# Optimization experiments

Hardware: AMD Instinct MI355X
Metric: run time of the kernel (lower is better)

Reference implementation:

```python
import jax, jax.numpy as jnp
import numpy as np

N, E, B, D, L = 100000, 600000, 128, 128, 3
BOT = 64
EPS = 1e-5


def _forward(query_x, corpus_x, gin_eps, mlp_W1, mlp_b1, mlp_W2, mlp_b2, bn_gamma, bn_beta,
             pool_G1, pool_g1b, pool_G2, pool_g2b, pool_Wm,
             int_G1, int_g1b, int_G2, int_g2b, int_F1, int_f1b, int_F2, int_f2b,
             sc_G1, sc_g1b, sc_G2, sc_g2b, sc_F1, sc_f1b, sc_F2, sc_f2b,
             query_edge_index, query_graph_idx, corpus_edge_index, corpus_graph_idx, num_graphs):
    def gin(x, ei, l):
        # GINConv: sum of source-node features into targets, plus (1+eps)*self
        agg = jax.ops.segment_sum(x[ei[0]], ei[1], num_segments=x.shape[0])
        h = (1.0 + gin_eps[l]) * x + agg
        h = jax.nn.relu(h @ mlp_W1[l] + mlp_b1[l]) @ mlp_W2[l] + mlp_b2[l]
        mu = h.mean(axis=0)
        var = ((h - mu) ** 2).mean(axis=0)  # biased var (BatchNorm training mode)
        h = (h - mu) * jax.lax.rsqrt(var + EPS) * bn_gamma[l] + bn_beta[l]
        return jax.nn.relu(h)  # dropout p=0.0

    def pool(x, gidx, l):
        coef = jnp.tanh(jax.nn.relu(x @ pool_G1[l] + pool_g1b[l]) @ pool_G2[l] + pool_g2b[l])
        s = (coef + 1.0) * x
        sums = jax.ops.segment_sum(s, gidx, num_segments=num_graphs)
        cnt = jax.ops.segment_sum(jnp.ones((x.shape[0],), x.dtype), gidx, num_segments=num_graphs)
        mean = sums / cnt[:, None]
        gc = jnp.tanh(mean @ pool_Wm[l])  # [B, D]
        node_coef = jax.nn.sigmoid(jnp.sum(s * gc[gidx], axis=1))  # [N]
        return jax.ops.segment_sum(node_coef[:, None] * s, gidx, num_segments=num_graphs)

    def interact(q, c, l):
        comb = jnp.concatenate([q, c], axis=1)  # [B, 2D]
        coef = jax.nn.sigmoid(jax.nn.relu(comb @ int_G1[l] + int_g1b[l]) @ int_G2[l] + int_g2b[l])
        sc = (coef + 1.0) * comb
        return jax.nn.relu(jax.nn.relu(sc @ int_F1[l] + int_f1b[l]) @ int_F2[l] + int_f2b[l])

    qx, cx = query_x, corpus_x
    feats = []
    for l in range(gin_eps.shape[0]):
        qx = gin(qx, query_edge_index, l)
        cx = gin(cx, corpus_edge_index, l)
        feats.append(interact(pool(qx, query_graph_idx, l), pool(cx, corpus_graph_idx, l), l))
    f = jnp.concatenate(feats, axis=1)  # [B, sum(filters)//2]
    coef = jax.nn.sigmoid(jax.nn.relu(f @ sc_G1 + sc_g1b) @ sc_G2 + sc_g2b)
    sf = (coef + 1.0) * f
    return (jax.nn.relu(sf @ sc_F1 + sc_f1b) @ sc_F2 + sc_f2b).squeeze(-1)  # [B]


def setup_inputs() -> dict:
    key = jax.random.key(0)
    kit = iter(jax.random.split(key, 64))
    def nrm(shape, s=0.05):
        return jax.random.normal(next(kit), shape, jnp.float32) * s
    C, R, OUT, AGG, RG = 2 * D, (2 * D) // 4, D // 2, (3 * D) // 2, ((3 * D) // 2) // 4
    inp = {
        "query_x": nrm((N, D), 1.0),
        "query_edge_index": jax.random.randint(next(kit), (2, E), 0, N),
        "query_graph_idx": jnp.sort(jax.random.randint(next(kit), (N,), 0, B)),
        "corpus_x": nrm((N, D), 1.0),
        "corpus_edge_index": jax.random.randint(next(kit), (2, E), 0, N),
        "corpus_graph_idx": jnp.sort(jax.random.randint(next(kit), (N,), 0, B)),
        "num_graphs": B,
        "gin_eps": jnp.zeros((L,), jnp.float32),
        "mlp_W1": nrm((L, D, D)), "mlp_b1": jnp.zeros((L, D)),
        "mlp_W2": nrm((L, D, D)), "mlp_b2": jnp.zeros((L, D)),
        "bn_gamma": jnp.ones((L, D)), "bn_beta": jnp.zeros((L, D)),
        "pool_G1": nrm((L, D, D // 4)), "pool_g1b": jnp.zeros((L, D // 4)),
        "pool_G2": nrm((L, D // 4, D)), "pool_g2b": jnp.zeros((L, D)),
        "pool_Wm": nrm((L, D, D)),
        "int_G1": nrm((L, C, R)), "int_g1b": jnp.zeros((L, R)),
        "int_G2": nrm((L, R, C)), "int_g2b": jnp.zeros((L, C)),
        "int_F1": nrm((L, C, C)), "int_f1b": jnp.zeros((L, C)),
        "int_F2": nrm((L, C, OUT)), "int_f2b": jnp.zeros((L, OUT)),
        "sc_G1": nrm((AGG, RG)), "sc_g1b": jnp.zeros((RG,)),
        "sc_G2": nrm((RG, AGG)), "sc_g2b": jnp.zeros((AGG,)),
        "sc_F1": nrm((AGG, BOT)), "sc_f1b": jnp.zeros((BOT,)),
        "sc_F2": nrm((BOT, 1)), "sc_f2b": jnp.zeros((1,)),
    }
    return inp


def reference(query_x, query_edge_index, query_graph_idx, corpus_x, corpus_edge_index, corpus_graph_idx,
              num_graphs, gin_eps, mlp_W1, mlp_b1, mlp_W2, mlp_b2, bn_gamma, bn_beta,
              pool_G1, pool_g1b, pool_G2, pool_g2b, pool_Wm,
              int_G1, int_g1b, int_G2, int_g2b, int_F1, int_f1b, int_F2, int_f2b,
              sc_G1, sc_g1b, sc_G2, sc_g2b, sc_F1, sc_f1b, sc_F2, sc_f2b):
    return _forward(query_x, corpus_x, gin_eps, mlp_W1, mlp_b1, mlp_W2, mlp_b2, bn_gamma, bn_beta,
                    pool_G1, pool_g1b, pool_G2, pool_g2b, pool_Wm,
                    int_G1, int_g1b, int_G2, int_g2b, int_F1, int_f1b, int_F2, int_f2b,
                    sc_G1, sc_g1b, sc_G2, sc_g2b, sc_F1, sc_f1b, sc_F2, sc_f2b,
                    query_edge_index, query_graph_idx, corpus_edge_index, corpus_graph_idx, num_graphs)
```

## Files before the change

kernel.cpp:

```cpp
#include <hip/hip_runtime.h>
#include <hip/hip_bf16.h>

constexpr int NN  = 100000;
constexpr int NN2 = 200000;
constexpr int NE  = 600000;
constexpr int NB  = 128;
constexpr int D   = 128;
constexpr int NL  = 3;
constexpr int CAP = 48;
constexpr int MT_TOT = NN2 / 16;
constexpr int MT_Q   = NN / 16;

constexpr int PREP_CSR   = (2 * NE + 255) / 256;
constexpr int PREP_WPREP = 1956;
constexpr int PREP_CNT   = 64;
constexpr int PREP_TOT   = PREP_CSR + PREP_WPREP + PREP_CNT;

constexpr int NCSEG_BLK = 1024;

typedef __bf16 bf16x8 __attribute__((ext_vector_type(8)));
typedef float f32x4 __attribute__((ext_vector_type(4)));
typedef unsigned short us8 __attribute__((ext_vector_type(8)));

__device__ __forceinline__ float sigmoidf_(float x) { return 1.0f / (1.0f + __expf(-x)); }
__device__ __forceinline__ unsigned short f2b(float f) {
    __hip_bfloat16 h = __float2bfloat16(f);
    return __builtin_bit_cast(unsigned short, h);
}
__device__ __forceinline__ float b2f(unsigned short u) {
    __hip_bfloat16 h = __builtin_bit_cast(__hip_bfloat16, u);
    return __bfloat162float(h);
}
__device__ __forceinline__ bf16x8 ldfrag(const unsigned short* p) {
    return __builtin_bit_cast(bf16x8, *(const us8*)p);
}

__device__ __forceinline__ void ncseg_body(int vbid, int nstream_blocks,
                                           const unsigned short* __restrict__ S,
                                           const int* __restrict__ gq, const int* __restrict__ gc,
                                           const float* __restrict__ gcb,
                                           float* __restrict__ dq, float* __restrict__ dc) {
    int stream = vbid * 4 + (threadIdx.x >> 6);
    int lane = threadIdx.x & 63;
    int nstream = nstream_blocks * 4;
    int per = (NN2 + nstream - 1) / nstream;
    int r0 = stream * per;
    int r1 = min(r0 + per, NN2);
    if (r0 >= r1) return;
    float a0 = 0.f, a1 = 0.f;
    int cur = (r0 < NN) ? gq[r0] : 128 + gc[r0 - NN];
    for (int r = r0; r < r1; ++r) {
        int g = (r < NN) ? gq[r] : 128 + gc[r - NN];
        if (g != cur) {
            float* base = (cur < 128) ? (dq + cur * D) : (dc + (cur - 128) * D);
            atomicAdd(&base[lane * 2], a0);
            atomicAdd(&base[lane * 2 + 1], a1);
            a0 = 0.f; a1 = 0.f; cur = g;
        }
        ushort2 sv = *(const ushort2*)&S[(size_t)r * D + lane * 2];
        float2 gv = *(const float2*)&gcb[(size_t)g * D + lane * 2];
        float v0 = b2f(sv.x), v1 = b2f(sv.y);
        float p = v0 * gv.x + v1 * gv.y;
#pragma unroll
        for (int off = 1; off < 64; off <<= 1) p += __shfl_xor(p, off, 64);
        float nc = sigmoidf_(p);
        a0 += nc * v0; a1 += nc * v1;
    }
    float* base = (cur < 128) ? (dq + cur * D) : (dc + (cur - 128) * D);
    atomicAdd(&base[lane * 2], a0);
    atomicAdd(&base[lane * 2 + 1], a1);
}

__device__ __forceinline__ void gather_bf16_body(int vbid,
                                                 const unsigned short* __restrict__ xb,
                                                 unsigned short* __restrict__ z,
                                                 const int* __restrict__ deg, const int* __restrict__ bucket,
                                                 float e) {
    int r = vbid * 16 + (threadIdx.x >> 4);
    int c8 = threadIdx.x & 15;
    float a[8];
    us8 v = *(const us8*)(xb + (size_t)r * D + c8 * 8);
#pragma unroll
    for (int j = 0; j < 8; ++j) a[j] = e * b2f(v[j]);
    int d = deg[r]; d = (d < CAP) ? d : CAP;
    const int* bk = bucket + (size_t)r * CAP;
    int i = 0;
    for (; i + 4 <= d; i += 4) {
        int s0 = bk[i], s1 = bk[i + 1], s2 = bk[i + 2], s3 = bk[i + 3];
        us8 u0 = *(const us8*)(xb + (size_t)s0 * D + c8 * 8);
        us8 u1 = *(const us8*)(xb + (size_t)s1 * D + c8 * 8);
        us8 u2 = *(const us8*)(xb + (size_t)s2 * D + c8 * 8);
        us8 u3 = *(const us8*)(xb + (size_t)s3 * D + c8 * 8);
#pragma unroll
        for (int j = 0; j < 8; ++j)
            a[j] += b2f(u0[j]) + b2f(u1[j]) + b2f(u2[j]) + b2f(u3[j]);
    }
    for (; i < d; ++i) {
        int s0 = bk[i];
        us8 u0 = *(const us8*)(xb + (size_t)s0 * D + c8 * 8);
#pragma unroll
        for (int j = 0; j < 8; ++j) a[j] += b2f(u0[j]);
    }
    us8 o;
#pragma unroll
    for (int j = 0; j < 8; ++j) o[j] = f2b(a[j]);
    *(us8*)(z + (size_t)r * D + c8 * 8) = o;
}

__global__ __launch_bounds__(256) void k_prep(
    const int* __restrict__ qei, const int* __restrict__ cei,
    int* __restrict__ deg, int* __restrict__ bucket,
    const float* mW1, const float* mW2, const float* pG1, const float* pG2,
    const float* iG1, const float* iG2, const float* iF1, const float* iF2,
    const float* sG1, const float* sG2, const float* sF1,
    unsigned short* W1t, unsigned short* W2t, unsigned short* G1t, unsigned short* G2t,
    unsigned short* iG1t, unsigned short* iG2t, unsigned short* iF1t, unsigned short* iF2t,
    unsigned short* sG1t, unsigned short* sG2t, unsigned short* sF1t,
    const int* __restrict__ gq, const int* __restrict__ gc, float* __restrict__ cnt) {
    if (blockIdx.x < PREP_CSR) {
        int e = blockIdx.x * 256 + threadIdx.x;
        int src, dst;
        if (e < NE) {
            src = qei[e]; dst = qei[NE + e];
        } else if (e < 2 * NE) {
            src = cei[e - NE] + NN; dst = cei[NE + (e - NE)] + NN;
        } else return;
        int pos = atomicAdd(&deg[dst], 1);
        if (pos < CAP) bucket[(size_t)dst * CAP + pos] = src;
        return;
    }
    if (blockIdx.x < PREP_CSR + PREP_WPREP) {
        int i = (blockIdx.x - PREP_CSR) * 256 + threadIdx.x;
#define SEG(CNT, KK, NN_, SRC, DST)                                              \
        if (i < (CNT)) {                                                         \
            int l = i / ((KK) * (NN_)), r = i % ((KK) * (NN_));                  \
            int n = r / (KK), k = r % (KK);                                      \
            DST[i] = f2b(SRC[(size_t)l * (KK) * (NN_) + (size_t)k * (NN_) + n]); \
            return;                                                              \
        }                                                                        \
        i -= (CNT);
        SEG(49152, 128, 128, mW1, W1t)
        SEG(49152, 128, 128, mW2, W2t)
        SEG(12288, 128, 32, pG1, G1t)
        SEG(12288, 32, 128, pG2, G2t)
        SEG(49152, 256, 64, iG1, iG1t)
        SEG(49152, 64, 256, iG2, iG2t)
        SEG(196608, 256, 256, iF1, iF1t)
        SEG(49152, 256, 64, iF2, iF2t)
        SEG(9216, 192, 48, sG1, sG1t)
        if (i < 12288) {
            int n = i / 64, k = i % 64;
            sG2t[i] = (k < 48) ? f2b(sG2[(size_t)k * 192 + n]) : (unsigned short)0;
            return;
        }
        i -= 12288;
        SEG(12288, 192, 64, sF1, sF1t)
#undef SEG
        return;
    }
    {
        __shared__ float h[256];
        int vb = blockIdx.x - (PREP_CSR + PREP_WPREP);
        for (int i = threadIdx.x; i < 256; i += 256) h[i] = 0.f;
        __syncthreads();
        int total = PREP_CNT * 256;
        int tid = vb * 256 + threadIdx.x;
        int per = (NN2 + total - 1) / total;
        int r0 = tid * per, r1 = min(r0 + per, NN2);
        if (r0 < r1) {
            int cur = (r0 < NN) ? gq[r0] : 128 + gc[r0 - NN];
            float c = 0.f;
            for (int r = r0; r < r1; ++r) {
                int g = (r < NN) ? gq[r] : 128 + gc[r - NN];
                if (g != cur) { atomicAdd(&h[cur], c); c = 0.f; cur = g; }
                c += 1.f;
            }
            atomicAdd(&h[cur], c);
        }
        __syncthreads();
        for (int i = threadIdx.x; i < 256; i += 256)
            if (h[i] != 0.f) atomicAdd(&cnt[i], h[i]);
    }
}

__global__ __launch_bounds__(256) void k_gather0(const float* __restrict__ qx, const float* __restrict__ cx,
                                                 unsigned short* __restrict__ z,
                                                 const int* __restrict__ deg, const int* __restrict__ bucket,
                                                 const float* __restrict__ eps_p) {
    int r = blockIdx.x * 16 + (threadIdx.x >> 4);
    int c8 = threadIdx.x & 15;
    float e = 1.0f + eps_p[0];
    float a[8];
    const float* base = (r < NN) ? qx : cx;
    int off = (r < NN) ? 0 : NN;
    float4 v0 = *(const float4*)(base + (size_t)(r - off) * D + c8 * 8);
    float4 v1 = *(const float4*)(base + (size_t)(r - off) * D + c8 * 8 + 4);
    a[0] = e * v0.x; a[1] = e * v0.y; a[2] = e * v0.z; a[3] = e * v0.w;
    a[4] = e * v1.x; a[5] = e * v1.y; a[6] = e * v1.z; a[7] = e * v1.w;
    int d = deg[r]; d = (d < CAP) ? d : CAP;
    const int* bk = bucket + (size_t)r * CAP;
    int i = 0;
    for (; i + 4 <= d; i += 4) {
        int s0 = bk[i], s1 = bk[i + 1], s2 = bk[i + 2], s3 = bk[i + 3];
        const float* p0 = base + (size_t)(s0 - off) * D + c8 * 8;
        const float* p1 = base + (size_t)(s1 - off) * D + c8 * 8;
        const float* p2 = base + (size_t)(s2 - off) * D + c8 * 8;
        const float* p3 = base + (size_t)(s3 - off) * D + c8 * 8;
        float4 w0 = *(const float4*)p0, w0b = *(const float4*)(p0 + 4);
        float4 w1 = *(const float4*)p1, w1b = *(const float4*)(p1 + 4);
        float4 w2 = *(const float4*)p2, w2b = *(const float4*)(p2 + 4);
        float4 w3 = *(const float4*)p3, w3b = *(const float4*)(p3 + 4);
        a[0] += w0.x + w1.x + w2.x + w3.x; a[1] += w0.y + w1.y + w2.y + w3.y;
        a[2] += w0.z + w1.z + w2.z + w3.z; a[3] += w0.w + w1.w + w2.w + w3.w;
        a[4] += w0b.x + w1b.x + w2b.x + w3b.x; a[5] += w0b.y + w1b.y + w2b.y + w3b.y;
        a[6] += w0b.z + w1b.z + w2b.z + w3b.z; a[7] += w0b.w + w1b.w + w2b.w + w3b.w;
    }
    for (; i < d; ++i) {
        int s0 = bk[i];
        const float* p0 = base + (size_t)(s0 - off) * D + c8 * 8;
        float4 w0 = *(const float4*)p0, w0b = *(const float4*)(p0 + 4);
        a[0] += w0.x; a[1] += w0.y; a[2] += w0.z; a[3] += w0.w;
        a[4] += w0b.x; a[5] += w0b.y; a[6] += w0b.z; a[7] += w0b.w;
    }
    us8 o;
#pragma unroll
    for (int j = 0; j < 8; ++j) o[j] = f2b(a[j]);
    *(us8*)(z + (size_t)r * D + c8 * 8) = o;
}

__global__ __launch_bounds__(256) void k_gncseg(const unsigned short* __restrict__ xb,
                                                unsigned short* __restrict__ z,
                                                const int* __restrict__ deg, const int* __restrict__ bucket,
                                                const float* __restrict__ eps_p, int l,
                                                const unsigned short* __restrict__ S,
                                                const int* __restrict__ gq, const int* __restrict__ gcix,
                                                const float* __restrict__ gcb,
                                                float* __restrict__ dq, float* __restrict__ dc) {
    if (blockIdx.x < NCSEG_BLK) {
        ncseg_body(blockIdx.x, NCSEG_BLK, S, gq, gcix, gcb, dq, dc);
    } else {
        float e = 1.0f + eps_p[l];
        gather_bf16_body(blockIdx.x - NCSEG_BLK, xb, z, deg, bucket, e);
    }
}

__global__ __launch_bounds__(256) void k_ncseg(const unsigned short* __restrict__ S,
                                               const int* __restrict__ gq, const int* __restrict__ gc,
                                               const float* __restrict__ gcb,
                                               float* __restrict__ dq, float* __restrict__ dc) {
    ncseg_body(blockIdx.x, NCSEG_BLK, S, gq, gc, gcb, dq, dc);
}

constexpr int HSTR = 136;
__global__ __launch_bounds__(256, 2) void k_mlp(unsigned short* zh,
                                                const unsigned short* __restrict__ W1t,
                                                const unsigned short* __restrict__ W2t,
                                                const float* __restrict__ b1,
                                                const float* __restrict__ b2,
                                                float* __restrict__ stat) {
    __shared__ unsigned short hb[2][2][16 * HSTR];
    __shared__ float red[512];
    int wave = threadIdx.x >> 6, lane = threadIdx.x & 63;
    int col16 = lane & 15, quad = lane >> 4;
    int g = wave >> 1, half = wave & 1;
    bf16x8 bf1[4][4], bf2[4][4];
    float bb1[4], bb2[4];
#pragma unroll
    for (int t = 0; t < 4; ++t) {
        int c = half * 64 + t * 16 + col16;
        bb1[t] = b1[c]; bb2[t] = b2[c];
#pragma unroll
        for (int kc = 0; kc < 4; ++kc) {
            bf1[t][kc] = ldfrag(W1t + (size_t)c * D + kc * 32 + quad * 8);
            bf2[t][kc] = ldfrag(W2t + (size_t)c * D + kc * 32 + quad * 8);
        }
    }
    float cs[2][4] = {{0.f,0.f,0.f,0.f},{0.f,0.f,0.f,0.f}};
    float cq[2][4] = {{0.f,0.f,0.f,0.f},{0.f,0.f,0.f,0.f}};
    int groups = gridDim.x * 2;
    int iters = (MT_TOT + groups - 1) / groups;
    bf16x8 zf[4];
    {
        int mt = blockIdx.x * 2 + g;
        const unsigned short* Ap = zh + ((size_t)((mt < MT_TOT) ? mt : 0) * 16 + col16) * D + quad * 8;
#pragma unroll
        for (int kc = 0; kc < 4; ++kc) zf[kc] = ldfrag(Ap + kc * 32);
    }
    for (int n = 0; n < iters; ++n) {
        int mt = blockIdx.x * 2 + g + n * groups;
        bool act = (mt < MT_TOT);
        int pp = n & 1;
        unsigned short* hbuf = hb[pp][g];
        bf16x8 zn[4];
        {
            int mtn = blockIdx.x * 2 + g + (n + 1) * groups;
            const unsigned short* Apn = zh + ((size_t)((mtn < MT_TOT) ? mtn : 0) * 16 + col16) * D + quad * 8;
#pragma unroll
            for (int kc = 0; kc < 4; ++kc) zn[kc] = ldfrag(Apn + kc * 32);
        }
        {
            f32x4 acc[4];
#pragma unroll
            for (int t = 0; t < 4; ++t) acc[t] = (f32x4){0.f, 0.f, 0.f, 0.f};
#pragma unroll
            for (int kc = 0; kc < 4; ++kc) {
#pragma unroll
                for (int t = 0; t < 4; ++t)
                    acc[t] = __builtin_amdgcn_mfma_f32_16x16x32_bf16(zf[kc], bf1[t][kc], acc[t], 0, 0, 0);
            }
#pragma unroll
            for (int t = 0; t < 4; ++t) {
                int c = half * 64 + t * 16 + col16;
#pragma unroll
                for (int r = 0; r < 4; ++r)
                    hbuf[(quad * 4 + r) * HSTR + c] = f2b(fmaxf(acc[t][r] + bb1[t], 0.f));
            }
        }
        __syncthreads();
        {
            f32x4 acc[4];
#pragma unroll
            for (int t = 0; t < 4; ++t) acc[t] = (f32x4){0.f, 0.f, 0.f, 0.f};
#pragma unroll
            for (int kc = 0; kc < 4; ++kc) {
                bf16x8 af = ldfrag(&hbuf[col16 * HSTR + kc * 32 + quad * 8]);
#pragma unroll
                for (int t = 0; t < 4; ++t)
                    acc[t] = __builtin_amdgcn_mfma_f32_16x16x32_bf16(af, bf2[t][kc], acc[t], 0, 0, 0);
            }
            if (act) {
                int side = (mt < MT_Q) ? 0 : 1;
#pragma unroll
                for (int t = 0; t < 4; ++t) {
                    int c = half * 64 + t * 16 + col16;
#pragma unroll
                    for (int r = 0; r < 4; ++r) {
                        int m = mt * 16 + quad * 4 + r;
                        float v = acc[t][r] + bb2[t];
                        zh[(size_t)m * D + c] = f2b(v);
                        cs[side][t] += v; cq[side][t] += v * v;
                    }
                }
            }
        }
#pragma unroll
        for (int kc = 0; kc < 4; ++kc) zf[kc] = zn[kc];
    }
    for (int i = threadIdx.x; i < 512; i += 256) red[i] = 0.f;
    __syncthreads();
#pragma unroll
    for (int t = 0; t < 4; ++t) {
        int c = half * 64 + t * 16 + col16;
#pragma unroll
        for (int side = 0; side < 2; ++side) {
            atomicAdd(&red[side * 256 + c], cs[side][t]);
            atomicAdd(&red[side * 256 + 128 + c], cq[side][t]);
        }
    }
    __syncthreads();
    for (int i = threadIdx.x; i < 512; i += 256) atomicAdd(&stat[i], red[i]);
}

__global__ __launch_bounds__(256, 3) void k_pool(const unsigned short* __restrict__ H,
                                                 const unsigned short* __restrict__ G1t,
                                                 const unsigned short* __restrict__ G2t,
                                                 const float* __restrict__ b1,
                                                 const float* __restrict__ b2,
                                                 const float* __restrict__ stat,
                                                 const float* __restrict__ gamma,
                                                 const float* __restrict__ beta,
                                                 const int* __restrict__ gq, const int* __restrict__ gcix,
                                                 unsigned short* __restrict__ Xo,
                                                 unsigned short* __restrict__ S,
                                                 float* __restrict__ seg_sum) {
    __shared__ float sc_s[256], sh_s[256];
    __shared__ unsigned short xt[4][16 * HSTR];
    __shared__ unsigned short t2t[4][16 * 40];
    {
        int t = threadIdx.x, side = t >> 7, c = t & 127;
        const float invN = 1.0f / (float)NN;
        float mu = stat[side * 256 + c] * invN;
        float var = fmaxf(stat[side * 256 + 128 + c] * invN - mu * mu, 0.f);
        float inv = rsqrtf(var + 1e-5f);
        float s = gamma[c] * inv;
        sc_s[t] = s;
        sh_s[t] = beta[c] - mu * s;
    }
    __syncthreads();
    int wave = threadIdx.x >> 6, lane = threadIdx.x & 63;
    int col16 = lane & 15, quad = lane >> 4;
    unsigned short* xtile = xt[wave];
    unsigned short* t2tile = t2t[wave];
    int nwaves = gridDim.x * 4;
    int per = (MT_TOT + nwaves - 1) / nwaves;
    int wid = blockIdx.x * 4 + wave;
    int mt0 = wid * per, mt1 = min(mt0 + per, MT_TOT);
    if (mt0 >= mt1) return;

    float bb1[2], bb2[8];
#pragma unroll
    for (int t = 0; t < 2; ++t) bb1[t] = b1[t * 16 + col16];
#pragma unroll
    for (int t = 0; t < 8; ++t) bb2[t] = b2[t * 16 + col16];
    float sacc[8] = {0.f, 0.f, 0.f, 0.f, 0.f, 0.f, 0.f, 0.f};
    int curg = -1;
    for (int mt = mt0; mt < mt1; ++mt) {
        int side = (mt < MT_Q) ? 0 : 1;
        const float* scp = sc_s + side * 128;
        const float* shp = sh_s + side * 128;
        const unsigned short* Hp = H + ((size_t)mt * 16 + col16) * D + quad * 8;
        unsigned short* Xp = Xo + ((size_t)mt * 16 + col16) * D + quad * 8;
        f32x4 acc1[2];
#pragma unroll
        for (int t = 0; t < 2; ++t) acc1[t] = (f32x4){0.f, 0.f, 0.f, 0.f};
#pragma unroll
        for (int kc = 0; kc < 4; ++kc) {
            us8 hv = *(const us8*)(Hp + kc * 32);
            int k0 = kc * 32 + quad * 8;
            float4 s0 = *(const float4*)&scp[k0], s1 = *(const float4*)&scp[k0 + 4];
            float4 h0 = *(const float4*)&shp[k0], h1 = *(const float4*)&shp[k0 + 4];
            us8 xv;
            xv[0] = f2b(fmaxf(b2f(hv[0]) * s0.x + h0.x, 0.f));
            xv[1] = f2b(fmaxf(b2f(hv[1]) * s0.y + h0.y, 0.f));
            xv[2] = f2b(fmaxf(b2f(hv[2]) * s0.z + h0.z, 0.f));
            xv[3] = f2b(fmaxf(b2f(hv[3]) * s0.w + h0.w, 0.f));
            xv[4] = f2b(fmaxf(b2f(hv[4]) * s1.x + h1.x, 0.f));
            xv[5] = f2b(fmaxf(b2f(hv[5]) * s1.y + h1.y, 0.f));
            xv[6] = f2b(fmaxf(b2f(hv[6]) * s1.z + h1.z, 0.f));
            xv[7] = f2b(fmaxf(b2f(hv[7]) * s1.w + h1.w, 0.f));
            *(us8*)(Xp + kc * 32) = xv;
            *(us8*)(xtile + col16 * HSTR + k0) = xv;
            bf16x8 af = __builtin_bit_cast(bf16x8, xv);
#pragma unroll
            for (int t = 0; t < 2; ++t) {
                bf16x8 wf = ldfrag(G1t + (size_t)(t * 16 + col16) * D + kc * 32 + quad * 8);
                acc1[t] = __builtin_amdgcn_mfma_f32_16x16x32_bf16(af, wf, acc1[t], 0, 0, 0);
            }
        }
#pragma unroll
        for (int t = 0; t < 2; ++t) {
            int c = t * 16 + col16;
#pragma unroll
            for (int r = 0; r < 4; ++r)
                t2tile[(quad * 4 + r) * 40 + c] = f2b(fmaxf(acc1[t][r] + bb1[t], 0.f));
        }
        bf16x8 af2 = ldfrag(t2tile + col16 * 40 + quad * 8);
        f32x4 acc2[8];
#pragma unroll
        for (int t = 0; t < 8; ++t) {
            bf16x8 wf = ldfrag(G2t + (size_t)(t * 16 + col16) * 32 + quad * 8);
            acc2[t] = (f32x4){0.f, 0.f, 0.f, 0.f};
            acc2[t] = __builtin_amdgcn_mfma_f32_16x16x32_bf16(af2, wf, acc2[t], 0, 0, 0);
        }
#pragma unroll
        for (int r = 0; r < 4; ++r) {
            int m = mt * 16 + quad * 4 + r;
            int g = (m < NN) ? gq[m] : 128 + gcix[m - NN];
            if (g != curg) {
                if (curg >= 0) {
#pragma unroll
                    for (int t = 0; t < 8; ++t) {
                        atomicAdd(&seg_sum[(size_t)curg * D + t * 16 + col16], sacc[t]);
                        sacc[t] = 0.f;
                    }
                }
                curg = g;
            }
#pragma unroll
            for (int t = 0; t < 8; ++t) {
                int c = t * 16 + col16;
                float v = (tanhf(acc2[t][r] + bb2[t]) + 1.f) * b2f(xtile[(quad * 4 + r) * HSTR + c]);
                S[(size_t)m * D + c] = f2b(v);
                sacc[t] += v;
            }
        }
    }
    if (curg >= 0) {
#pragma unroll
        for (int t = 0; t < 8; ++t)
            atomicAdd(&seg_sum[(size_t)curg * D + t * 16 + col16], sacc[t]);
    }
}

__global__ void k_gc(float* __restrict__ sums, const float* __restrict__ cnt,
                     const float* __restrict__ Wm, float* __restrict__ gc) {
    __shared__ float m[D];
    int b = blockIdx.x, j = threadIdx.x;
    m[j] = sums[b * D + j] / cnt[b];
    sums[b * D + j] = 0.f;
    __syncthreads();
    float a = 0.f;
#pragma unroll 8
    for (int i = 0; i < D; ++i) a += m[i] * Wm[i * D + j];
    gc[b * D + j] = tanhf(a);
}

constexpr int LSTR = 264;
__global__ __launch_bounds__(256) void k_interact(const float* __restrict__ pooled,
                                                  const unsigned short* __restrict__ iG1t, const float* __restrict__ ig1b,
                                                  const unsigned short* __restrict__ iG2t, const float* __restrict__ ig2b,
                                                  const unsigned short* __restrict__ iF1t, const float* __restrict__ if1b,
                                                  const unsigned short* __restrict__ iF2t, const float* __restrict__ if2b,
                                                  unsigned short* __restrict__ featsb) {
    __shared__ unsigned short bufC[16 * LSTR];
    __shared__ unsigned short bufA[16 * LSTR];
    __shared__ unsigned short bufB[16 * LSTR];
    int t = threadIdx.x, wave = t >> 6, lane = t & 63;
    int col16 = lane & 15, quad = lane >> 4;
    int pg = blockIdx.x & 7, l = blockIdx.x >> 3;
    int p0 = pg * 16;
    {
        int r = t >> 4, c0 = (t & 15) * 16;
        const float* src = (c0 < 128)
            ? (pooled + (size_t)l * NB * D + (size_t)(p0 + r) * D + c0)
            : (pooled + (size_t)(NL + l) * NB * D + (size_t)(p0 + r) * D + (c0 - 128));
#pragma unroll
        for (int j = 0; j < 16; ++j) bufC[r * LSTR + c0 + j] = f2b(src[j]);
    }
    __syncthreads();
    {
        f32x4 acc = (f32x4){0.f, 0.f, 0.f, 0.f};
        int n = wave * 16 + col16;
#pragma unroll
        for (int kc = 0; kc < 8; ++kc) {
            bf16x8 af = ldfrag(&bufC[col16 * LSTR + kc * 32 + quad * 8]);
            bf16x8 bfr = ldfrag(iG1t + ((size_t)l * 64 + n) * 256 + kc * 32 + quad * 8);
            acc = __builtin_amdgcn_mfma_f32_16x16x32_bf16(af, bfr, acc, 0, 0, 0);
        }
        float bb = ig1b[(size_t)l * 64 + n];
#pragma unroll
        for (int r = 0; r < 4; ++r)
            bufA[(quad * 4 + r) * LSTR + n] = f2b(fmaxf(acc[r] + bb, 0.f));
    }
    __syncthreads();
    {
        f32x4 acc[4];
#pragma unroll
        for (int tt = 0; tt < 4; ++tt) acc[tt] = (f32x4){0.f, 0.f, 0.f, 0.f};
#pragma unroll
        for (int kc = 0; kc < 2; ++kc) {
            bf16x8 af = ldfrag(&bufA[col16 * LSTR + kc * 32 + quad * 8]);
#pragma unroll
            for (int tt = 0; tt < 4; ++tt) {
                int n = wave * 64 + tt * 16 + col16;
                bf16x8 bfr = ldfrag(iG2t + ((size_t)l * 256 + n) * 64 + kc * 32 + quad * 8);
                acc[tt] = __builtin_amdgcn_mfma_f32_16x16x32_bf16(af, bfr, acc[tt], 0, 0, 0);
            }
        }
#pragma unroll
        for (int tt = 0; tt < 4; ++tt) {
            int n = wave * 64 + tt * 16 + col16;
            float bb = ig2b[(size_t)l * 256 + n];
#pragma unroll
            for (int r = 0; r < 4; ++r) {
                int row = quad * 4 + r;
                float s = (sigmoidf_(acc[tt][r] + bb) + 1.f) * b2f(bufC[row * LSTR + n]);
                bufB[row * LSTR + n] = f2b(s);
            }
        }
    }
    __syncthreads();
    {
        f32x4 acc[4];
#pragma unroll
        for (int tt = 0; tt < 4; ++tt) acc[tt] = (f32x4){0.f, 0.f, 0.f, 0.f};
#pragma unroll
        for (int kc = 0; kc < 8; ++kc) {
            bf16x8 af = ldfrag(&bufB[col16 * LSTR + kc * 32 + quad * 8]);
#pragma unroll
            for (int tt = 0; tt < 4; ++tt) {
                int n = wave * 64 + tt * 16 + col16;
                bf16x8 bfr = ldfrag(iF1t + (size_t)l * 256 * 256 + (size_t)n * 256 + kc * 32 + quad * 8);
                acc[tt] = __builtin_amdgcn_mfma_f32_16x16x32_bf16(af, bfr, acc[tt], 0, 0, 0);
            }
        }
#pragma unroll
        for (int tt = 0; tt < 4; ++tt) {
            int n = wave * 64 + tt * 16 + col16;
            float bb = if1b[(size_t)l * 256 + n];
#pragma unroll
            for (int r = 0; r < 4; ++r)
                bufA[(quad * 4 + r) * LSTR + n] = f2b(fmaxf(acc[tt][r] + bb, 0.f));
        }
    }
    __syncthreads();
    {
        f32x4 acc = (f32x4){0.f, 0.f, 0.f, 0.f};
        int n = wave * 16 + col16;
#pragma unroll
        for (int kc = 0; kc < 8; ++kc) {
            bf16x8 af = ldfrag(&bufA[col16 * LSTR + kc * 32 + quad * 8]);
            bf16x8 bfr = ldfrag(iF2t + ((size_t)l * 64 + n) * 256 + kc * 32 + quad * 8);
            acc = __builtin_amdgcn_mfma_f32_16x16x32_bf16(af, bfr, acc, 0, 0, 0);
        }
        float bb = if2b[(size_t)l * 64 + n];
#pragma unroll
        for (int r = 0; r < 4; ++r)
            featsb[(size_t)(p0 + quad * 4 + r) * 192 + l * 64 + n] = f2b(fmaxf(acc[r] + bb, 0.f));
    }
}

__global__ __launch_bounds__(256) void k_score(const unsigned short* __restrict__ featsb,
                                               const unsigned short* __restrict__ sG1t, const float* __restrict__ sg1b,
                                               const unsigned short* __restrict__ sG2t, const float* __restrict__ sg2b,
                                               const unsigned short* __restrict__ sF1t, const float* __restrict__ sf1b,
                                               const float* __restrict__ sF2, const float* __restrict__ sf2b,
                                               float* __restrict__ out) {
    __shared__ unsigned short bufF[16 * 200];
    __shared__ unsigned short bufA[16 * LSTR];
    __shared__ unsigned short bufB[16 * LSTR];
    __shared__ float redf[16 * 65];
    int t = threadIdx.x, wave = t >> 6, lane = t & 63;
    int col16 = lane & 15, quad = lane >> 4;
    int p0 = blockIdx.x * 16;
    {
        int r = t >> 4, c0 = (t & 15) * 12;
#pragma unroll
        for (int j = 0; j < 12; ++j)
            bufF[r * 200 + c0 + j] = featsb[(size_t)(p0 + r) * 192 + c0 + j];
    }
    __syncthreads();
    if (wave < 3) {
        f32x4 acc = (f32x4){0.f, 0.f, 0.f, 0.f};
        int n = wave * 16 + col16;
#pragma unroll
        for (int kc = 0; kc < 6; ++kc) {
            bf16x8 af = ldfrag(&bufF[col16 * 200 + kc * 32 + quad * 8]);
            bf16x8 bfr = ldfrag(sG1t + (size_t)n * 192 + kc * 32 + quad * 8);
            acc = __builtin_amdgcn_mfma_f32_16x16x32_bf16(af, bfr, acc, 0, 0, 0);
        }
        float bb = sg1b[n];
#pragma unroll
        for (int r = 0; r < 4; ++r)
            bufA[(quad * 4 + r) * LSTR + n] = f2b(fmaxf(acc[r] + bb, 0.f));
    } else {
        int row = lane >> 2, c = 48 + (lane & 3) * 4;
#pragma unroll
        for (int j = 0; j < 4; ++j) bufA[row * LSTR + c + j] = 0;
    }
    __syncthreads();
    {
        f32x4 acc[3];
#pragma unroll
        for (int tt = 0; tt < 3; ++tt) acc[tt] = (f32x4){0.f, 0.f, 0.f, 0.f};
#pragma unroll
        for (int kc = 0; kc < 2; ++kc) {
            bf16x8 af = ldfrag(&bufA[col16 * LSTR + kc * 32 + quad * 8]);
#pragma unroll
            for (int tt = 0; tt < 3; ++tt) {
                int n = wave * 48 + tt * 16 + col16;
                bf16x8 bfr = ldfrag(sG2t + (size_t)n * 64 + kc * 32 + quad * 8);
                acc[tt] = __builtin_amdgcn_mfma_f32_16x16x32_bf16(af, bfr, acc[tt], 0, 0, 0);
            }
        }
#pragma unroll
        for (int tt = 0; tt < 3; ++tt) {
            int n = wave * 48 + tt * 16 + col16;
            float bb = sg2b[n];
#pragma unroll
            for (int r = 0; r < 4; ++r) {
                int row = quad * 4 + r;
                float s = (sigmoidf_(acc[tt][r] + bb) + 1.f) * b2f(bufF[row * 200 + n]);
                bufB[row * LSTR + n] = f2b(s);
            }
        }
    }
    __syncthreads();
    {
        f32x4 acc = (f32x4){0.f, 0.f, 0.f, 0.f};
        int n = wave * 16 + col16;
#pragma unroll
        for (int kc = 0; kc < 6; ++kc) {
            bf16x8 af = ldfrag(&bufB[col16 * LSTR + kc * 32 + quad * 8]);
            bf16x8 bfr = ldfrag(sF1t + (size_t)n * 192 + kc * 32 + quad * 8);
            acc = __builtin_amdgcn_mfma_f32_16x16x32_bf16(af, bfr, acc, 0, 0, 0);
        }
        float bb = sf1b[n], w2 = sF2[n];
#pragma unroll
        for (int r = 0; r < 4; ++r)
            redf[(quad * 4 + r) * 65 + n] = fmaxf(acc[r] + bb, 0.f) * w2;
    }
    __syncthreads();
    if (t < 16) {
        float s = 0.f;
#pragma unroll 8
        for (int i = 0; i < 64; ++i) s += redf[t * 65 + i];
        out[p0 + t] = s + sf2b[0];
    }
}

extern "C" void kernel_launch(void* const* d_in, const int* in_sizes, int n_in,
                              void* d_out, int out_size, void* d_ws, size_t ws_size,
                              hipStream_t stream) {
    const float* query_x   = (const float*)d_in[0];
    const int*   query_ei  = (const int*)d_in[1];
    const int*   query_gi  = (const int*)d_in[2];
    const float* corpus_x  = (const float*)d_in[3];
    const int*   corpus_ei = (const int*)d_in[4];
    const int*   corpus_gi = (const int*)d_in[5];
    const float* gin_eps   = (const float*)d_in[7];
    const float* mlp_W1    = (const float*)d_in[8];
    const float* mlp_b1    = (const float*)d_in[9];
    const float* mlp_W2    = (const float*)d_in[10];
    const float* mlp_b2    = (const float*)d_in[11];
    const float* bn_gamma  = (const float*)d_in[12];
    const float* bn_beta   = (const float*)d_in[13];
    const float* pool_G1   = (const float*)d_in[14];
    const float* pool_g1b  = (const float*)d_in[15];
    const float* pool_G2   = (const float*)d_in[16];
    const float* pool_g2b  = (const float*)d_in[17];
    const float* pool_Wm   = (const float*)d_in[18];
    const float* int_G1    = (const float*)d_in[19];
    const float* int_g1b   = (const float*)d_in[20];
    const float* int_G2    = (const float*)d_in[21];
    const float* int_g2b   = (const float*)d_in[22];
    const float* int_F1    = (const float*)d_in[23];
    const float* int_f1b   = (const float*)d_in[24];
    const float* int_F2    = (const float*)d_in[25];
    const float* int_f2b   = (const float*)d_in[26];
    const float* sc_G1     = (const float*)d_in[27];
    const float* sc_g1b    = (const float*)d_in[28];
    const float* sc_G2     = (const float*)d_in[29];
    const float* sc_g2b    = (const float*)d_in[30];
    const float* sc_F1     = (const float*)d_in[31];
    const float* sc_f1b    = (const float*)d_in[32];
    const float* sc_F2     = (const float*)d_in[33];
    const float* sc_f2b    = (const float*)d_in[34];
    float* out = (float*)d_out;

    unsigned short* Zb  = (unsigned short*)d_ws;
    unsigned short* Xb  = Zb + (size_t)NN2 * D;
    unsigned short* Sb  = Xb + (size_t)NN2 * D;
    unsigned short* featsb = Sb + (size_t)NN2 * D;
    unsigned short* W1t = featsb + 128 * 192;
    unsigned short* W2t = W1t + NL * D * D;
    unsigned short* G1t = W2t + NL * D * D;
    unsigned short* G2t = G1t + NL * 32 * D;
    unsigned short* iG1t = G2t + NL * D * 32;
    unsigned short* iG2t = iG1t + NL * 64 * 256;
    unsigned short* iF1t = iG2t + NL * 256 * 64;
    unsigned short* iF2t = iF1t + NL * 256 * 256;
    unsigned short* sG1t = iF2t + NL * 64 * 256;
    unsigned short* sG2t = sG1t + 48 * 192;
    unsigned short* sF1t = sG2t + 192 * 64;
    int* deg    = (int*)(sF1t + 64 * 192);
    int* bucket = deg + NN2;
    float* bn_stat  = (float*)(bucket + (size_t)NN2 * CAP);
    float* seg_sum  = bn_stat + NL * 512;
    float* seg_cnt  = seg_sum + 256 * D;
    float* gcb      = seg_cnt + 256;
    float* pooled   = gcb + 256 * D;

    hipMemsetAsync(deg, 0, NN2 * sizeof(int), stream);
    hipMemsetAsync(bn_stat, 0, NL * 512 * sizeof(float), stream);
    hipMemsetAsync(pooled, 0, 2 * NL * NB * D * sizeof(float), stream);
    hipMemsetAsync(seg_cnt, 0, 256 * sizeof(float), stream);
    hipMemsetAsync(seg_sum, 0, 256 * D * sizeof(float), stream);

    k_prep<<<PREP_TOT, 256, 0, stream>>>(query_ei, corpus_ei, deg, bucket,
                                         mlp_W1, mlp_W2, pool_G1, pool_G2,
                                         int_G1, int_G2, int_F1, int_F2,
                                         sc_G1, sc_G2, sc_F1,
                                         W1t, W2t, G1t, G2t, iG1t, iG2t, iF1t, iF2t,
                                         sG1t, sG2t, sF1t,
                                         query_gi, corpus_gi, seg_cnt);

    for (int l = 0; l < NL; ++l) {
        if (l == 0)
            k_gather0<<<MT_TOT, 256, 0, stream>>>(query_x, corpus_x, Zb, deg, bucket, gin_eps);
        else
            k_gncseg<<<NCSEG_BLK + MT_TOT, 256, 0, stream>>>(
                Xb, Zb, deg, bucket, gin_eps, l,
                Sb, query_gi, corpus_gi, gcb,
                pooled + (size_t)(l - 1) * NB * D,
                pooled + (size_t)(NL + l - 1) * NB * D);
        k_mlp<<<1024, 256, 0, stream>>>(Zb, W1t + (size_t)l * D * D, W2t + (size_t)l * D * D,
                                        mlp_b1 + l * D, mlp_b2 + l * D, bn_stat + l * 512);
        k_pool<<<782, 256, 0, stream>>>(Zb, G1t + (size_t)l * 32 * D, G2t + (size_t)l * D * 32,
                                        pool_g1b + l * 32, pool_g2b + l * D,
                                        bn_stat + l * 512, bn_gamma + l * D, bn_beta + l * D,
                                        query_gi, corpus_gi, Xb, Sb, seg_sum);
        k_gc<<<256, D, 0, stream>>>(seg_sum, seg_cnt, pool_Wm + (size_t)l * D * D, gcb);
    }
    k_ncseg<<<NCSEG_BLK, 256, 0, stream>>>(Sb, query_gi, corpus_gi, gcb,
                                           pooled + (size_t)(NL - 1) * NB * D,
                                           pooled + (size_t)(2 * NL - 1) * NB * D);
    k_interact<<<24, 256, 0, stream>>>(pooled, iG1t, int_g1b, iG2t, int_g2b,
                                       iF1t, int_f1b, iF2t, int_f2b, featsb);
    k_score<<<8, 256, 0, stream>>>(featsb, sG1t, sc_g1b, sG2t, sc_g2b,
                                   sF1t, sc_f1b, sc_F2, sc_f2b, out);
}
```

Baseline: 988.3 us.

## Apply BatchNorm+ReLU on the fly in gather instead of materializing X

The pool kernel no longer writes the normalized activation X. Instead block 0 exports the per-column BN scale and shift, and the next layer's gather kernel reads the raw MLP output H and applies scale, shift, ReLU and bf16 rounding per neighbor load. Buffers ping-pong between Zb and Xb so the gather can read H while writing its aggregate. This removes one full write of a 200k×128 bf16 array per layer, at the cost of extra ALU work for every gathered neighbor (about 7 per node).

```diff
diff --git a/kernel.cpp b/kernel.cpp
--- a/kernel.cpp
+++ b/kernel.cpp
@@ -71,35 +71,52 @@
     atomicAdd(&base[lane * 2 + 1], a1);
 }
 
-__device__ __forceinline__ void gather_bf16_body(int vbid,
-                                                 const unsigned short* __restrict__ xb,
-                                                 unsigned short* __restrict__ z,
-                                                 const int* __restrict__ deg, const int* __restrict__ bucket,
-                                                 float e) {
+__device__ __forceinline__ float xval_(unsigned short hu, float sc, float sh) {
+    return b2f(f2b(fmaxf(b2f(hu) * sc + sh, 0.f)));
+}
+__device__ __forceinline__ void gather_h_body(int vbid,
+                                              const unsigned short* __restrict__ hb_,
+                                              unsigned short* __restrict__ z,
+                                              const int* __restrict__ deg, const int* __restrict__ bucket,
+                                              float e, const float* __restrict__ bnsc) {
     int r = vbid * 16 + (threadIdx.x >> 4);
     int c8 = threadIdx.x & 15;
+    int side = (r < NN) ? 0 : 1;
+    const float* bp = bnsc + side * 256;
+    float sc[8], sh[8];
+    {
+        float4 a0 = *(const float4*)(bp + c8 * 8);
+        float4 a1 = *(const float4*)(bp + c8 * 8 + 4);
+        float4 b0 = *(const float4*)(bp + 128 + c8 * 8);
+        float4 b1 = *(const float4*)(bp + 128 + c8 * 8 + 4);
+        sc[0] = a0.x; sc[1] = a0.y; sc[2] = a0.z; sc[3] = a0.w;
+        sc[4] = a1.x; sc[5] = a1.y; sc[6] = a1.z; sc[7] = a1.w;
+        sh[0] = b0.x; sh[1] = b0.y; sh[2] = b0.z; sh[3] = b0.w;
+        sh[4] = b1.x; sh[5] = b1.y; sh[6] = b1.z; sh[7] = b1.w;
+    }
     float a[8];
-    us8 v = *(const us8*)(xb + (size_t)r * D + c8 * 8);
-#pragma unroll
-    for (int j = 0; j < 8; ++j) a[j] = e * b2f(v[j]);
+    us8 v = *(const us8*)(hb_ + (size_t)r * D + c8 * 8);
+#pragma unroll
+    for (int j = 0; j < 8; ++j) a[j] = e * xval_(v[j], sc[j], sh[j]);
     int d = deg[r]; d = (d < CAP) ? d : CAP;
     const int* bk = bucket + (size_t)r * CAP;
     int i = 0;
     for (; i + 4 <= d; i += 4) {
         int s0 = bk[i], s1 = bk[i + 1], s2 = bk[i + 2], s3 = bk[i + 3];
-        us8 u0 = *(const us8*)(xb + (size_t)s0 * D + c8 * 8);
-        us8 u1 = *(const us8*)(xb + (size_t)s1 * D + c8 * 8);
-        us8 u2 = *(const us8*)(xb + (size_t)s2 * D + c8 * 8);
-        us8 u3 = *(const us8*)(xb + (size_t)s3 * D + c8 * 8);
+        us8 u0 = *(const us8*)(hb_ + (size_t)s0 * D + c8 * 8);
+        us8 u1 = *(const us8*)(hb_ + (size_t)s1 * D + c8 * 8);
+        us8 u2 = *(const us8*)(hb_ + (size_t)s2 * D + c8 * 8);
+        us8 u3 = *(const us8*)(hb_ + (size_t)s3 * D + c8 * 8);
 #pragma unroll
         for (int j = 0; j < 8; ++j)
-            a[j] += b2f(u0[j]) + b2f(u1[j]) + b2f(u2[j]) + b2f(u3[j]);
+            a[j] += xval_(u0[j], sc[j], sh[j]) + xval_(u1[j], sc[j], sh[j])
+                  + xval_(u2[j], sc[j], sh[j]) + xval_(u3[j], sc[j], sh[j]);
     }
     for (; i < d; ++i) {
         int s0 = bk[i];
-        us8 u0 = *(const us8*)(xb + (size_t)s0 * D + c8 * 8);
-#pragma unroll
-        for (int j = 0; j < 8; ++j) a[j] += b2f(u0[j]);
+        us8 u0 = *(const us8*)(hb_ + (size_t)s0 * D + c8 * 8);
+#pragma unroll
+        for (int j = 0; j < 8; ++j) a[j] += xval_(u0[j], sc[j], sh[j]);
     }
     us8 o;
 #pragma unroll
@@ -228,10 +245,11 @@
     *(us8*)(z + (size_t)r * D + c8 * 8) = o;
 }
 
-__global__ __launch_bounds__(256) void k_gncseg(const unsigned short* __restrict__ xb,
+__global__ __launch_bounds__(256) void k_gncseg(const unsigned short* __restrict__ hb_,
                                                 unsigned short* __restrict__ z,
                                                 const int* __restrict__ deg, const int* __restrict__ bucket,
                                                 const float* __restrict__ eps_p, int l,
+                                                const float* __restrict__ bnsc,
                                                 const unsigned short* __restrict__ S,
                                                 const int* __restrict__ gq, const int* __restrict__ gcix,
                                                 const float* __restrict__ gcb,
@@ -240,7 +258,7 @@
         ncseg_body(blockIdx.x, NCSEG_BLK, S, gq, gcix, gcb, dq, dc);
     } else {
         float e = 1.0f + eps_p[l];
-        gather_bf16_body(blockIdx.x - NCSEG_BLK, xb, z, deg, bucket, e);
+        gather_h_body(blockIdx.x - NCSEG_BLK, hb_, z, deg, bucket, e, bnsc);
     }
 }
 
@@ -370,9 +388,9 @@
                                                  const float* __restrict__ gamma,
                                                  const float* __restrict__ beta,
                                                  const int* __restrict__ gq, const int* __restrict__ gcix,
-                                                 unsigned short* __restrict__ Xo,
                                                  unsigned short* __restrict__ S,
-                                                 float* __restrict__ seg_sum) {
+                                                 float* __restrict__ seg_sum,
+                                                 float* __restrict__ bnsc_out) {
     __shared__ float sc_s[256], sh_s[256];
     __shared__ unsigned short xt[4][16 * HSTR];
     __shared__ unsigned short t2t[4][16 * 40];
@@ -385,6 +403,10 @@
         float s = gamma[c] * inv;
         sc_s[t] = s;
         sh_s[t] = beta[c] - mu * s;
+        if (blockIdx.x == 0) {
+            bnsc_out[side * 256 + c] = s;
+            bnsc_out[side * 256 + 128 + c] = beta[c] - mu * s;
+        }
     }
     __syncthreads();
     int wave = threadIdx.x >> 6, lane = threadIdx.x & 63;
@@ -409,7 +431,6 @@
         const float* scp = sc_s + side * 128;
         const float* shp = sh_s + side * 128;
         const unsigned short* Hp = H + ((size_t)mt * 16 + col16) * D + quad * 8;
-        unsigned short* Xp = Xo + ((size_t)mt * 16 + col16) * D + quad * 8;
         f32x4 acc1[2];
 #pragma unroll
         for (int t = 0; t < 2; ++t) acc1[t] = (f32x4){0.f, 0.f, 0.f, 0.f};
@@ -428,7 +449,6 @@
             xv[5] = f2b(fmaxf(b2f(hv[5]) * s1.y + h1.y, 0.f));
             xv[6] = f2b(fmaxf(b2f(hv[6]) * s1.z + h1.z, 0.f));
             xv[7] = f2b(fmaxf(b2f(hv[7]) * s1.w + h1.w, 0.f));
-            *(us8*)(Xp + kc * 32) = xv;
             *(us8*)(xtile + col16 * HSTR + k0) = xv;
             bf16x8 af = __builtin_bit_cast(bf16x8, xv);
 #pragma unroll
@@ -750,6 +770,7 @@
     float* seg_cnt  = seg_sum + 256 * D;
     float* gcb      = seg_cnt + 256;
     float* pooled   = gcb + 256 * D;
+    float* bnsc     = pooled + 2 * NL * NB * D;
 
     hipMemsetAsync(deg, 0, NN2 * sizeof(int), stream);
     hipMemsetAsync(bn_stat, 0, NL * 512 * sizeof(float), stream);
@@ -765,21 +786,27 @@
                                          sG1t, sG2t, sF1t,
                                          query_gi, corpus_gi, seg_cnt);
 
+    unsigned short* cur = Zb;
     for (int l = 0; l < NL; ++l) {
-        if (l == 0)
+        if (l == 0) {
             k_gather0<<<MT_TOT, 256, 0, stream>>>(query_x, corpus_x, Zb, deg, bucket, gin_eps);
-        else
+            cur = Zb;
+        } else {
+            unsigned short* dst = (cur == Zb) ? Xb : Zb;
             k_gncseg<<<NCSEG_BLK + MT_TOT, 256, 0, stream>>>(
-                Xb, Zb, deg, bucket, gin_eps, l,
+                cur, dst, deg, bucket, gin_eps, l, bnsc + (size_t)(l - 1) * 512,
                 Sb, query_gi, corpus_gi, gcb,
                 pooled + (size_t)(l - 1) * NB * D,
                 pooled + (size_t)(NL + l - 1) * NB * D);
-        k_mlp<<<1024, 256, 0, stream>>>(Zb, W1t + (size_t)l * D * D, W2t + (size_t)l * D * D,
+            cur = dst;
+        }
+        k_mlp<<<1024, 256, 0, stream>>>(cur, W1t + (size_t)l * D * D, W2t + (size_t)l * D * D,
                                         mlp_b1 + l * D, mlp_b2 + l * D, bn_stat + l * 512);
-        k_pool<<<782, 256, 0, stream>>>(Zb, G1t + (size_t)l * 32 * D, G2t + (size_t)l * D * 32,
+        k_pool<<<782, 256, 0, stream>>>(cur, G1t + (size_t)l * 32 * D, G2t + (size_t)l * D * 32,
                                         pool_g1b + l * 32, pool_g2b + l * D,
                                         bn_stat + l * 512, bn_gamma + l * D, bn_beta + l * D,
-                                        query_gi, corpus_gi, Xb, Sb, seg_sum);
+                                        query_gi, corpus_gi, Sb, seg_sum,
+                                        bnsc + (size_t)l * 512);
         k_gc<<<256, D, 0, stream>>>(seg_sum, seg_cnt, pool_Wm + (size_t)l * D * D, gcb);
     }
     k_ncseg<<<NCSEG_BLK, 256, 0, stream>>>(Sb, query_gi, corpus_gi, gcb,
```

Result: no change. 986.7 us (-0.2%).
